# Performance work log

Hardware: AMD Instinct MI355X
Metric: run time of the kernel (lower is better)

Reference implementation:

```python
import jax, jax.numpy as jnp
import numpy as np

B, L, S, D, H = 2, 2048, 2048, 256, 8
HD = D // H  # per-head dim = 32
EPS = 1e-5


def _layernorm(x, g, b):
    m = jnp.mean(x, axis=-1, keepdims=True)
    v = jnp.mean(jnp.square(x - m), axis=-1, keepdims=True)
    return (x - m) * jax.lax.rsqrt(v + EPS) * g + b


def setup_inputs() -> dict:
    key = jax.random.key(0)
    ks = jax.random.split(key, 12)
    w = lambda k, o, i: jax.random.normal(k, (o, i), dtype=jnp.float32) * (1.0 / np.sqrt(i))
    return {
        "x": jax.random.normal(ks[0], (B, L, D), dtype=jnp.float32),
        "source": jax.random.normal(ks[1], (B, S, D), dtype=jnp.float32),
        "attn_factor": jax.random.uniform(ks[2], (B, L, S), dtype=jnp.float32),
        "Wq": w(ks[3], D, D),
        "Wk": w(ks[4], D, D),
        "Wv": w(ks[5], D, D),
        "Wm": w(ks[6], D, D),
        "W1": w(ks[7], 2 * D, 2 * D),
        "W2": w(ks[8], D, 2 * D),
        "g1": jnp.ones((D,), jnp.float32),
        "b1": jnp.zeros((D,), jnp.float32),
        "g2": jnp.ones((D,), jnp.float32),
        "b2": jnp.zeros((D,), jnp.float32),
    }


def reference(x, source, attn_factor, Wq, Wk, Wv, Wm, W1, W2, g1, b1, g2, b2):
    bs, l, d = x.shape
    s = source.shape[1]
    # projections (torch Linear: y = x @ W^T), split heads
    qw = (x @ Wq.T).reshape(bs, l, H, HD)       # [B,L,H,hd]
    kw = (source @ Wk.T).reshape(bs, s, H, HD)  # [B,S,H,hd]
    vw = (source @ Wv.T).reshape(bs, s, H, HD)  # [B,S,H,hd]
    # QK^T -> [B,L,S,H], scale, elementwise attn_factor, softmax over S
    a = jnp.einsum("nlhd,nshd->nlsh", qw, kw)
    a = a / np.sqrt(HD)
    a = a * attn_factor[:, :, :, None]
    a = jax.nn.softmax(a, axis=2)
    # AV -> [B,L,H,hd] -> merge heads
    o = jnp.einsum("nlsh,nshd->nlhd", a, vw).reshape(bs, l, d)
    message = o @ Wm.T
    message = _layernorm(message, g1, b1)
    h = jnp.concatenate([x, message], axis=2)       # [B,L,2D]
    h = jnp.maximum(h @ W1.T, 0.0)                  # ReLU MLP
    message = h @ W2.T                              # [B,L,D]
    message = _layernorm(message, g2, b2)
    return x + message
```

## Files before the change

### kernel.cpp

```cpp
#include <hip/hip_runtime.h>
#include <hip/hip_bf16.h>
#include <math.h>

#define B_  2
#define L_  2048
#define S_  2048
#define D_  256
#define H_  8
#define HD_ 32
#define ML_ (B_ * L_)
#define MS_ (B_ * S_)
#define NSPLIT 4
#define SCHUNK (S_ / NSPLIT)

typedef __attribute__((ext_vector_type(8))) short short8;
typedef __attribute__((ext_vector_type(4))) float f32x4;

__global__ __launch_bounds__(256) void convert_all(
    const float* __restrict__ x,  const float* __restrict__ src,
    const float* __restrict__ Wq, const float* __restrict__ Wk,
    const float* __restrict__ Wv, const float* __restrict__ Wm,
    const float* __restrict__ W1, const float* __restrict__ W2,
    __hip_bfloat16* xb,  __hip_bfloat16* srcb,
    __hip_bfloat16* Wqb, __hip_bfloat16* Wkb,
    __hip_bfloat16* Wvb, __hip_bfloat16* Wmb,
    __hip_bfloat16* W1b, __hip_bfloat16* W2b) {
    const size_t i4 = ((size_t)blockIdx.x * 256 + threadIdx.x) * 4;
    const float* sp; __hip_bfloat16* dp; size_t off;
    if      (i4 < 1048576) { sp = x;   dp = xb;   off = i4; }
    else if (i4 < 2097152) { sp = src; dp = srcb; off = i4 - 1048576; }
    else if (i4 < 2162688) { sp = Wq;  dp = Wqb;  off = i4 - 2097152; }
    else if (i4 < 2228224) { sp = Wk;  dp = Wkb;  off = i4 - 2162688; }
    else if (i4 < 2293760) { sp = Wv;  dp = Wvb;  off = i4 - 2228224; }
    else if (i4 < 2359296) { sp = Wm;  dp = Wmb;  off = i4 - 2293760; }
    else if (i4 < 2621440) { sp = W1;  dp = W1b;  off = i4 - 2359296; }
    else                   { sp = W2;  dp = W2b;  off = i4 - 2621440; }
    float4 v = *(const float4*)(sp + off);
    __hip_bfloat16 o0 = __float2bfloat16(v.x), o1 = __float2bfloat16(v.y);
    __hip_bfloat16 o2 = __float2bfloat16(v.z), o3 = __float2bfloat16(v.w);
    __hip_bfloat16* d = dp + off;
    d[0] = o0; d[1] = o1; d[2] = o2; d[3] = o3;
}

template <bool RELU, typename OutT>
__device__ __forceinline__ void gemm_body(const __hip_bfloat16* __restrict__ A,
                                          const __hip_bfloat16* __restrict__ A2,
                                          const __hip_bfloat16* __restrict__ Bm,
                                          OutT* __restrict__ C,
                                          int N, int K, int lda, int m0, int n0,
                                          float cscale,
                                          __hip_bfloat16 (&As)[64][72],
                                          __hip_bfloat16 (&Bs)[64][72]) {
    const int tid  = threadIdx.x;
    const int w    = tid >> 6;
    const int lane = tid & 63;
    const int colL = lane & 15;
    const int quad = lane >> 4;
    const int mh = (w & 1) * 32, nh = (w >> 1) * 32;
    const int srow = tid >> 3;
    const int scg  = (tid & 7) * 8;

    f32x4 acc[2][2] = {};

    auto loadA = [&](int p, int k0) -> short8 {
        const __hip_bfloat16* Asrc = A; int kk = k0;
        if (A2 && k0 >= 256) { Asrc = A2; kk = k0 - 256; }
        return *(const short8*)(Asrc + (size_t)(m0 + srow + p * 32) * lda + kk + scg);
    };
    auto loadB = [&](int p, int k0) -> short8 {
        return *(const short8*)(Bm + (size_t)(n0 + srow + p * 32) * K + k0 + scg);
    };

    short8 ra[2], rb[2];
#pragma unroll
    for (int p = 0; p < 2; ++p) { ra[p] = loadA(p, 0); rb[p] = loadB(p, 0); }

    for (int k0 = 0; k0 < K; k0 += 64) {
        __syncthreads();
#pragma unroll
        for (int p = 0; p < 2; ++p) {
            *(short8*)&As[srow + p * 32][scg] = ra[p];
            *(short8*)&Bs[srow + p * 32][scg] = rb[p];
        }
        __syncthreads();
        if (k0 + 64 < K) {
#pragma unroll
            for (int p = 0; p < 2; ++p) { ra[p] = loadA(p, k0 + 64); rb[p] = loadB(p, k0 + 64); }
        }
#pragma unroll
        for (int ks = 0; ks < 2; ++ks) {
            short8 af[2], bf[2];
#pragma unroll
            for (int i = 0; i < 2; ++i)
                af[i] = *(const short8*)&As[mh + i * 16 + colL][ks * 32 + quad * 8];
#pragma unroll
            for (int j = 0; j < 2; ++j)
                bf[j] = *(const short8*)&Bs[nh + j * 16 + colL][ks * 32 + quad * 8];
#pragma unroll
            for (int i = 0; i < 2; ++i)
#pragma unroll
                for (int j = 0; j < 2; ++j)
                    acc[i][j] = __builtin_amdgcn_mfma_f32_16x16x32_bf16(af[i], bf[j], acc[i][j], 0, 0, 0);
        }
    }
#pragma unroll
    for (int i = 0; i < 2; ++i)
#pragma unroll
        for (int r = 0; r < 4; ++r) {
            const size_t row = m0 + mh + i * 16 + quad * 4 + r;
#pragma unroll
            for (int j = 0; j < 2; ++j) {
                float v = acc[i][j][r] * cscale;
                if (RELU) v = fmaxf(v, 0.f);
                C[row * N + n0 + nh + j * 16 + colL] = (OutT)v;
            }
        }
}

__global__ __launch_bounds__(256) void proj_fused(const __hip_bfloat16* __restrict__ x_b,
                                                  const __hip_bfloat16* __restrict__ src_b,
                                                  const __hip_bfloat16* __restrict__ Wq_b,
                                                  const __hip_bfloat16* __restrict__ Wk_b,
                                                  const __hip_bfloat16* __restrict__ Wv_b,
                                                  __hip_bfloat16* __restrict__ Qb,
                                                  __hip_bfloat16* __restrict__ Kb,
                                                  __hip_bfloat16* __restrict__ Vtb) {
    __shared__ __hip_bfloat16 As[64][72];
    __shared__ __hip_bfloat16 Bs[64][72];
    const int id = blockIdx.x;
    if (id < 256) {
        gemm_body<false, __hip_bfloat16>(x_b, nullptr, Wq_b, Qb, 256, 256, 256,
                                         (id >> 2) * 64, (id & 3) * 64,
                                         0.17677669529663687f, As, Bs);
    } else if (id < 512) {
        const int t = id - 256;
        gemm_body<false, __hip_bfloat16>(src_b, nullptr, Wk_b, Kb, 256, 256, 256,
                                         (t >> 2) * 64, (t & 3) * 64, 1.f, As, Bs);
    } else {
        const int t = id - 512;
        const int b = t >> 7, u = t & 127;
        gemm_body<false, __hip_bfloat16>(Wv_b, nullptr, src_b + (size_t)b * S_ * D_,
                                         Vtb + (size_t)b * D_ * S_, S_, 256, 256,
                                         (u & 3) * 64, (u >> 2) * 64, 1.f, As, Bs);
    }
}

__global__ __launch_bounds__(256, 4) void attn_mfma(const __hip_bfloat16* __restrict__ Qb,
                                                    const __hip_bfloat16* __restrict__ Kb,
                                                    const __hip_bfloat16* __restrict__ Vtb,
                                                    const float* __restrict__ F,
                                                    __hip_bfloat16* __restrict__ Op,
                                                    float* __restrict__ Ll) {
    const int tid  = threadIdx.x;
    const int w    = tid >> 6;
    const int lane = tid & 63;
    const int colL = lane & 15;
    const int quad = lane >> 4;

    const int b     = blockIdx.z >> 2;
    const int split = blockIdx.z & 3;
    const int h     = blockIdx.y;
    const int qw    = blockIdx.x * 64 + w * 16;

    __shared__ __hip_bfloat16 Ks[128][40];
    __shared__ __hip_bfloat16 Vs[32][136];
    __shared__ __hip_bfloat16 Pw[4][16][72];

    const short8 aq = *(const short8*)(Qb + ((size_t)(b * L_ + qw + colL)) * D_ + h * HD_ + quad * 8);

    float lsum[4] = {0.f, 0.f, 0.f, 0.f};
    f32x4 o0 = {0.f, 0.f, 0.f, 0.f}, o1 = {0.f, 0.f, 0.f, 0.f};

    const int kr = tid >> 2, kc = (tid & 3) * 8;
    const int vr = tid >> 3, vc = (tid & 7) * 8;
    const __hip_bfloat16* kst = Kb + ((size_t)(b * S_ + kr)) * D_ + h * HD_ + kc;
    const __hip_bfloat16* vst = Vtb + (size_t)b * D_ * S_ + ((size_t)(h * HD_ + vr)) * S_ + vc;
    const float* fbase = F + ((size_t)(b * L_ + qw + quad * 4)) * S_ + colL;

    const int sbeg = split * SCHUNK, send = sbeg + SCHUNK;
    short8 rk[2], rv[2];
#pragma unroll
    for (int p = 0; p < 2; ++p) {
        rk[p] = *(const short8*)(kst + (size_t)(sbeg + p * 64) * D_);
        rv[p] = *(const short8*)(vst + sbeg + p * 64);
    }

    for (int s0 = sbeg; s0 < send; s0 += 128) {
        __syncthreads();
        *(short8*)&Ks[kr][kc]        = rk[0];
        *(short8*)&Ks[kr + 64][kc]   = rk[1];
        *(short8*)&Vs[vr][vc]        = rv[0];
        *(short8*)&Vs[vr][vc + 64]   = rv[1];
        __syncthreads();
        if (s0 + 128 < send) {
#pragma unroll
            for (int p = 0; p < 2; ++p) {
                rk[p] = *(const short8*)(kst + (size_t)(s0 + 128 + p * 64) * D_);
                rv[p] = *(const short8*)(vst + s0 + 128 + p * 64);
            }
        }
#pragma unroll
        for (int hs = 0; hs < 2; ++hs) {
            const int sh = s0 + hs * 64;
            f32x4 cc[4];
#pragma unroll
            for (int n = 0; n < 4; ++n) {
                short8 kf = *(const short8*)&Ks[hs * 64 + n * 16 + colL][quad * 8];
                f32x4 z = {0.f, 0.f, 0.f, 0.f};
                cc[n] = __builtin_amdgcn_mfma_f32_16x16x32_bf16(aq, kf, z, 0, 0, 0);
            }
#pragma unroll
            for (int n = 0; n < 4; ++n)
#pragma unroll
                for (int r = 0; r < 4; ++r) {
                    float fv = fbase[(size_t)r * S_ + sh + n * 16];
                    float p = __expf(cc[n][r] * fv);
                    lsum[r] += p;
                    Pw[w][quad * 4 + r][n * 16 + colL] = __float2bfloat16(p);
                }
            short8 a0 = *(const short8*)(&Pw[w][colL][quad * 8]);
            short8 a1 = *(const short8*)(&Pw[w][colL][32 + quad * 8]);
#pragma unroll
            for (int ks = 0; ks < 2; ++ks) {
                short8 ap = ks ? a1 : a0;
#pragma unroll
                for (int nt = 0; nt < 2; ++nt) {
                    short8 vf = *(const short8*)&Vs[nt * 16 + colL][hs * 64 + ks * 32 + quad * 8];
                    if (nt == 0) o0 = __builtin_amdgcn_mfma_f32_16x16x32_bf16(ap, vf, o0, 0, 0, 0);
                    else         o1 = __builtin_amdgcn_mfma_f32_16x16x32_bf16(ap, vf, o1, 0, 0, 0);
                }
            }
        }
    }

#pragma unroll
    for (int r = 0; r < 4; ++r) {
        float t = lsum[r];
        t += __shfl_xor(t, 1);
        t += __shfl_xor(t, 2);
        t += __shfl_xor(t, 4);
        t += __shfl_xor(t, 8);
        lsum[r] = t;
    }

#pragma unroll
    for (int r = 0; r < 4; ++r) {
        const size_t row = (size_t)(b * L_ + qw + quad * 4 + r);
        const size_t po = ((size_t)split * ML_ + row) * D_ + h * HD_;
        Op[po + colL]      = __float2bfloat16(o0[r]);
        Op[po + 16 + colL] = __float2bfloat16(o1[r]);
        if (colL == 0)
            Ll[((size_t)split * H_ + h) * ML_ + row] = lsum[r];
    }
}

__global__ __launch_bounds__(256) void mlp_fused(const __hip_bfloat16* __restrict__ Opart,
                                                 const float* __restrict__ Ll,
                                                 const __hip_bfloat16* __restrict__ x_b,
                                                 const __hip_bfloat16* __restrict__ Wm_b,
                                                 const __hip_bfloat16* __restrict__ W1_b,
                                                 const __hip_bfloat16* __restrict__ W2_b,
                                                 const float* __restrict__ g1,
                                                 const float* __restrict__ b1,
                                                 const float* __restrict__ g2,
                                                 const float* __restrict__ b2,
                                                 const float* __restrict__ x,
                                                 float* __restrict__ out) {
    __shared__ __hip_bfloat16 Bs[256][72];
    __shared__ __hip_bfloat16 As[16][72];
    __shared__ __hip_bfloat16 Acat[16][520];
    __shared__ __hip_bfloat16 Hs[16][520];
    __shared__ float gs[256], bs_[256];
    __shared__ float stats[4][16][2];
    __shared__ float Linv[16][8];

    const int tid  = threadIdx.x;
    const int w    = tid >> 6;
    const int lane = tid & 63;
    const int colL = lane & 15;
    const int quad = lane >> 4;
    const int nh   = w * 64;
    const int m0   = blockIdx.x * 16;
    const int srow = tid >> 3;
    const int scg  = (tid & 7) * 8;

    gs[tid] = g1[tid]; bs_[tid] = b1[tid];
    if (tid < 128) {
        const int row = tid >> 3, hh = tid & 7;
        float t = 0.f;
#pragma unroll
        for (int s = 0; s < NSPLIT; ++s)
            t += Ll[((size_t)s * H_ + hh) * ML_ + m0 + row];
        Linv[row][hh] = 1.f / t;
    }
    {
        const int xr = tid >> 4, xc = (tid & 15) * 16;
        *(short8*)&Acat[xr][xc]     = *(const short8*)(x_b + (size_t)(m0 + xr) * 256 + xc);
        *(short8*)&Acat[xr][xc + 8] = *(const short8*)(x_b + (size_t)(m0 + xr) * 256 + xc + 8);
    }
    __syncthreads();

    f32x4 acc[4] = {};
    auto loadA1 = [&](int k0) -> short8 {
        const float inv = Linv[srow][(k0 + scg) >> 5];
        float a[8] = {};
#pragma unroll
        for (int s = 0; s < NSPLIT; ++s) {
            short8 v = *(const short8*)(Opart + ((size_t)s * ML_ + m0 + srow) * 256 + k0 + scg);
#pragma unroll
            for (int e = 0; e < 8; ++e) {
                union { short s16; __hip_bfloat16 h; } c; c.s16 = v[e];
                a[e] += __bfloat162float(c.h);
            }
        }
        short8 outv;
#pragma unroll
        for (int e = 0; e < 8; ++e) {
            union { __hip_bfloat16 h; short s16; } c;
            c.h = __float2bfloat16(a[e] * inv);
            outv[e] = c.s16;
        }
        return outv;
    };

    {
        short8 ra = {};
        if (srow < 16) ra = loadA1(0);
        short8 rb[8];
#pragma unroll
        for (int p = 0; p < 8; ++p)
            rb[p] = *(const short8*)(Wm_b + (size_t)(srow + p * 32) * 256 + scg);
        for (int k0 = 0; k0 < 256; k0 += 64) {
            __syncthreads();
            if (srow < 16) *(short8*)&As[srow][scg] = ra;
#pragma unroll
            for (int p = 0; p < 8; ++p)
                *(short8*)&Bs[srow + p * 32][scg] = rb[p];
            __syncthreads();
            if (k0 + 64 < 256) {
                if (srow < 16) ra = loadA1(k0 + 64);
#pragma unroll
                for (int p = 0; p < 8; ++p)
                    rb[p] = *(const short8*)(Wm_b + (size_t)(srow + p * 32) * 256 + k0 + 64 + scg);
            }
#pragma unroll
            for (int ks = 0; ks < 2; ++ks) {
                short8 af = *(const short8*)&As[colL][ks * 32 + quad * 8];
#pragma unroll
                for (int j = 0; j < 4; ++j) {
                    short8 bf = *(const short8*)&Bs[nh + j * 16 + colL][ks * 32 + quad * 8];
                    acc[j] = __builtin_amdgcn_mfma_f32_16x16x32_bf16(af, bf, acc[j], 0, 0, 0);
                }
            }
        }
    }
#pragma unroll
    for (int r = 0; r < 4; ++r) {
        float s = 0.f, q = 0.f;
#pragma unroll
        for (int j = 0; j < 4; ++j) { float v = acc[j][r]; s += v; q += v * v; }
        s += __shfl_xor(s, 1); q += __shfl_xor(q, 1);
        s += __shfl_xor(s, 2); q += __shfl_xor(q, 2);
        s += __shfl_xor(s, 4); q += __shfl_xor(q, 4);
        s += __shfl_xor(s, 8); q += __shfl_xor(q, 8);
        if (colL == 0) { stats[w][quad * 4 + r][0] = s; stats[w][quad * 4 + r][1] = q; }
    }
    __syncthreads();
#pragma unroll
    for (int r = 0; r < 4; ++r) {
        const int row = quad * 4 + r;
        const float S = stats[0][row][0] + stats[1][row][0] + stats[2][row][0] + stats[3][row][0];
        const float Q = stats[0][row][1] + stats[1][row][1] + stats[2][row][1] + stats[3][row][1];
        const float mean = S * (1.f / 256.f);
        const float rstd = rsqrtf(Q * (1.f / 256.f) - mean * mean + 1e-5f);
#pragma unroll
        for (int j = 0; j < 4; ++j) {
            const int col = nh + j * 16 + colL;
            Acat[row][256 + col] = __float2bfloat16((acc[j][r] - mean) * rstd * gs[col] + bs_[col]);
        }
    }
    __syncthreads();

#pragma unroll 1
    for (int nc = 0; nc < 2; ++nc) {
#pragma unroll
        for (int j = 0; j < 4; ++j) acc[j] = (f32x4){0.f, 0.f, 0.f, 0.f};
        short8 rb[8];
#pragma unroll
        for (int p = 0; p < 8; ++p)
            rb[p] = *(const short8*)(W1_b + (size_t)(nc * 256 + srow + p * 32) * 512 + scg);
        for (int k0 = 0; k0 < 512; k0 += 64) {
            __syncthreads();
#pragma unroll
            for (int p = 0; p < 8; ++p)
                *(short8*)&Bs[srow + p * 32][scg] = rb[p];
            __syncthreads();
            if (k0 + 64 < 512) {
#pragma unroll
                for (int p = 0; p < 8; ++p)
                    rb[p] = *(const short8*)(W1_b + (size_t)(nc * 256 + srow + p * 32) * 512 + k0 + 64 + scg);
            }
#pragma unroll
            for (int ks = 0; ks < 2; ++ks) {
                short8 af = *(const short8*)&Acat[colL][k0 + ks * 32 + quad * 8];
#pragma unroll
                for (int j = 0; j < 4; ++j) {
                    short8 bf = *(const short8*)&Bs[nh + j * 16 + colL][ks * 32 + quad * 8];
                    acc[j] = __builtin_amdgcn_mfma_f32_16x16x32_bf16(af, bf, acc[j], 0, 0, 0);
                }
            }
        }
#pragma unroll
        for (int r = 0; r < 4; ++r) {
            const int row = quad * 4 + r;
#pragma unroll
            for (int j = 0; j < 4; ++j) {
                const int col = nc * 256 + nh + j * 16 + colL;
                Hs[row][col] = __float2bfloat16(fmaxf(acc[j][r], 0.f));
            }
        }
    }
    gs[tid] = g2[tid]; bs_[tid] = b2[tid];
    __syncthreads();

#pragma unroll
    for (int j = 0; j < 4; ++j) acc[j] = (f32x4){0.f, 0.f, 0.f, 0.f};
    {
        short8 rb[8];
#pragma unroll
        for (int p = 0; p < 8; ++p)
            rb[p] = *(const short8*)(W2_b + (size_t)(srow + p * 32) * 512 + scg);
        for (int k0 = 0; k0 < 512; k0 += 64) {
            __syncthreads();
#pragma unroll
            for (int p = 0; p < 8; ++p)
                *(short8*)&Bs[srow + p * 32][scg] = rb[p];
            __syncthreads();
            if (k0 + 64 < 512) {
#pragma unroll
                for (int p = 0; p < 8; ++p)
                    rb[p] = *(const short8*)(W2_b + (size_t)(srow + p * 32) * 512 + k0 + 64 + scg);
            }
#pragma unroll
            for (int ks = 0; ks < 2; ++ks) {
                short8 af = *(const short8*)&Hs[colL][k0 + ks * 32 + quad * 8];
#pragma unroll
                for (int j = 0; j < 4; ++j) {
                    short8 bf = *(const short8*)&Bs[nh + j * 16 + colL][ks * 32 + quad * 8];
                    acc[j] = __builtin_amdgcn_mfma_f32_16x16x32_bf16(af, bf, acc[j], 0, 0, 0);
                }
            }
        }
    }
#pragma unroll
    for (int r = 0; r < 4; ++r) {
        float s = 0.f, q = 0.f;
#pragma unroll
        for (int j = 0; j < 4; ++j) { float v = acc[j][r]; s += v; q += v * v; }
        s += __shfl_xor(s, 1); q += __shfl_xor(q, 1);
        s += __shfl_xor(s, 2); q += __shfl_xor(q, 2);
        s += __shfl_xor(s, 4); q += __shfl_xor(q, 4);
        s += __shfl_xor(s, 8); q += __shfl_xor(q, 8);
        if (colL == 0) { stats[w][quad * 4 + r][0] = s; stats[w][quad * 4 + r][1] = q; }
    }
    __syncthreads();
#pragma unroll
    for (int r = 0; r < 4; ++r) {
        const int row = quad * 4 + r;
        const float S = stats[0][row][0] + stats[1][row][0] + stats[2][row][0] + stats[3][row][0];
        const float Q = stats[0][row][1] + stats[1][row][1] + stats[2][row][1] + stats[3][row][1];
        const float mean = S * (1.f / 256.f);
        const float rstd = rsqrtf(Q * (1.f / 256.f) - mean * mean + 1e-5f);
        const size_t grow = (size_t)(m0 + row) * 256;
#pragma unroll
        for (int j = 0; j < 4; ++j) {
            const int col = nh + j * 16 + colL;
            out[grow + col] = (acc[j][r] - mean) * rstd * gs[col] + bs_[col] + x[grow + col];
        }
    }
}

extern "C" void kernel_launch(void* const* d_in, const int* in_sizes, int n_in,
                              void* d_out, int out_size, void* d_ws, size_t ws_size,
                              hipStream_t stream) {
    (void)in_sizes; (void)n_in; (void)out_size; (void)ws_size;
    const float* x   = (const float*)d_in[0];
    const float* src = (const float*)d_in[1];
    const float* F   = (const float*)d_in[2];
    const float* Wq  = (const float*)d_in[3];
    const float* Wk  = (const float*)d_in[4];
    const float* Wv  = (const float*)d_in[5];
    const float* Wm  = (const float*)d_in[6];
    const float* W1  = (const float*)d_in[7];
    const float* W2  = (const float*)d_in[8];
    const float* g1  = (const float*)d_in[9];
    const float* b1  = (const float*)d_in[10];
    const float* g2  = (const float*)d_in[11];
    const float* b2  = (const float*)d_in[12];
    float* out = (float*)d_out;

    char* ws = (char*)d_ws;
    __hip_bfloat16* x_b   = (__hip_bfloat16*)(ws);
    __hip_bfloat16* src_b = (__hip_bfloat16*)(ws + (2u << 20));
    __hip_bfloat16* Wq_b  = (__hip_bfloat16*)(ws + (4u << 20));
    __hip_bfloat16* Wk_b  = (__hip_bfloat16*)(ws + (4u << 20) + 131072);
    __hip_bfloat16* Wv_b  = (__hip_bfloat16*)(ws + (4u << 20) + 2 * 131072);
    __hip_bfloat16* Wm_b  = (__hip_bfloat16*)(ws + (4u << 20) + 3 * 131072);
    __hip_bfloat16* W1_b  = (__hip_bfloat16*)(ws + (4u << 20) + 4 * 131072);
    __hip_bfloat16* W2_b  = (__hip_bfloat16*)(ws + (4u << 20) + 4 * 131072 + 524288);
    __hip_bfloat16* Qb   = (__hip_bfloat16*)(ws + (6u << 20));
    __hip_bfloat16* Kb   = (__hip_bfloat16*)(ws + (8u << 20));
    __hip_bfloat16* Vtb  = (__hip_bfloat16*)(ws + (10u << 20));
    __hip_bfloat16* Opart = (__hip_bfloat16*)(ws + (14u << 20));
    float* Ll  = (float*)(ws + (22u << 20));

    dim3 blk(256);
    convert_all<<<dim3(2688), blk, 0, stream>>>(x, src, Wq, Wk, Wv, Wm, W1, W2,
                                                x_b, src_b, Wq_b, Wk_b, Wv_b, Wm_b, W1_b, W2_b);
    proj_fused<<<dim3(1024), blk, 0, stream>>>(x_b, src_b, Wq_b, Wk_b, Wv_b, Qb, Kb, Vtb);
    attn_mfma<<<dim3(L_ / 64, H_, B_ * NSPLIT), blk, 0, stream>>>(Qb, Kb, Vtb, F, Opart, Ll);
    mlp_fused<<<dim3(ML_ / 16), blk, 0, stream>>>(Opart, Ll, x_b, Wm_b, W1_b, W2_b,
                                                  g1, b1, g2, b2, x, out);
}
```

Before: 163.0 us.

## Process two heads per attention block and XOR-swizzle shared-memory tiles

Each attention block now computes two adjacent heads, so each block loads the attn_factor values, a 64-wide K tile and the V tile once and uses them for both heads. This halves the number of passes over the large fp32 attn_factor tensor, which is likely the main memory traffic. Padded shared-memory arrays are replaced by XOR-swizzled layouts for K, V and P to avoid bank conflicts without padding. The change doubles accumulator and register use per thread, which may lower occupancy. The proj_fused grid also shrinks from 1024 to 768 blocks with no visible reason.

```diff
diff --git a/kernel.cpp b/kernel.cpp
--- a/kernel.cpp
+++ b/kernel.cpp
@@ -159,98 +159,116 @@
 
     const int b     = blockIdx.z >> 2;
     const int split = blockIdx.z & 3;
-    const int h     = blockIdx.y;
+    const int by    = blockIdx.y;
     const int qw    = blockIdx.x * 64 + w * 16;
 
-    __shared__ __hip_bfloat16 Ks[128][40];
-    __shared__ __hip_bfloat16 Vs[32][136];
-    __shared__ __hip_bfloat16 Pw[4][16][72];
-
-    const short8 aq = *(const short8*)(Qb + ((size_t)(b * L_ + qw + colL)) * D_ + h * HD_ + quad * 8);
-
-    float lsum[4] = {0.f, 0.f, 0.f, 0.f};
-    f32x4 o0 = {0.f, 0.f, 0.f, 0.f}, o1 = {0.f, 0.f, 0.f, 0.f};
-
-    const int kr = tid >> 2, kc = (tid & 3) * 8;
-    const int vr = tid >> 3, vc = (tid & 7) * 8;
-    const __hip_bfloat16* kst = Kb + ((size_t)(b * S_ + kr)) * D_ + h * HD_ + kc;
-    const __hip_bfloat16* vst = Vtb + (size_t)b * D_ * S_ + ((size_t)(h * HD_ + vr)) * S_ + vc;
+    __shared__ __hip_bfloat16 Ks[128][64];
+    __shared__ __hip_bfloat16 Vs[64][128];
+    __shared__ __hip_bfloat16 Pw[4][16][64];
+
+    short8 aq2[2];
+#pragma unroll
+    for (int h2 = 0; h2 < 2; ++h2)
+        aq2[h2] = *(const short8*)(Qb + ((size_t)(b * L_ + qw + colL)) * D_ +
+                                   by * 64 + h2 * 32 + quad * 8);
+
+    float lsum[2][4] = {};
+    f32x4 o[2][2] = {};
+
+    const int kr  = tid >> 3;
+    const int kc8 = tid & 7;
+    const int vr  = tid >> 2;
+    const int vc4 = tid & 3;
+    const __hip_bfloat16* kst = Kb + ((size_t)(b * S_ + kr)) * D_ + by * 64 + kc8 * 8;
+    const __hip_bfloat16* vst = Vtb + (size_t)b * D_ * S_ + ((size_t)(by * 64 + vr)) * S_ + vc4 * 8;
     const float* fbase = F + ((size_t)(b * L_ + qw + quad * 4)) * S_ + colL;
 
     const int sbeg = split * SCHUNK, send = sbeg + SCHUNK;
-    short8 rk[2], rv[2];
-#pragma unroll
-    for (int p = 0; p < 2; ++p) {
-        rk[p] = *(const short8*)(kst + (size_t)(sbeg + p * 64) * D_);
-        rv[p] = *(const short8*)(vst + sbeg + p * 64);
+    short8 rk[4], rv[4];
+#pragma unroll
+    for (int p = 0; p < 4; ++p) {
+        rk[p] = *(const short8*)(kst + (size_t)(sbeg + p * 32) * D_);
+        rv[p] = *(const short8*)(vst + sbeg + p * 32);
     }
 
     for (int s0 = sbeg; s0 < send; s0 += 128) {
         __syncthreads();
-        *(short8*)&Ks[kr][kc]        = rk[0];
-        *(short8*)&Ks[kr + 64][kc]   = rk[1];
-        *(short8*)&Vs[vr][vc]        = rv[0];
-        *(short8*)&Vs[vr][vc + 64]   = rv[1];
+#pragma unroll
+        for (int p = 0; p < 4; ++p) {
+            *(short8*)&Ks[p * 32 + kr][(kc8 ^ (kr & 7)) * 8]           = rk[p];
+            *(short8*)&Vs[vr][((p * 4 + vc4) ^ (vr & 7)) * 8]          = rv[p];
+        }
         __syncthreads();
         if (s0 + 128 < send) {
 #pragma unroll
-            for (int p = 0; p < 2; ++p) {
-                rk[p] = *(const short8*)(kst + (size_t)(s0 + 128 + p * 64) * D_);
-                rv[p] = *(const short8*)(vst + s0 + 128 + p * 64);
+            for (int p = 0; p < 4; ++p) {
+                rk[p] = *(const short8*)(kst + (size_t)(s0 + 128 + p * 32) * D_);
+                rv[p] = *(const short8*)(vst + s0 + 128 + p * 32);
             }
         }
 #pragma unroll
         for (int hs = 0; hs < 2; ++hs) {
             const int sh = s0 + hs * 64;
-            f32x4 cc[4];
-#pragma unroll
-            for (int n = 0; n < 4; ++n) {
-                short8 kf = *(const short8*)&Ks[hs * 64 + n * 16 + colL][quad * 8];
-                f32x4 z = {0.f, 0.f, 0.f, 0.f};
-                cc[n] = __builtin_amdgcn_mfma_f32_16x16x32_bf16(aq, kf, z, 0, 0, 0);
-            }
-#pragma unroll
-            for (int n = 0; n < 4; ++n)
-#pragma unroll
-                for (int r = 0; r < 4; ++r) {
-                    float fv = fbase[(size_t)r * S_ + sh + n * 16];
-                    float p = __expf(cc[n][r] * fv);
-                    lsum[r] += p;
-                    Pw[w][quad * 4 + r][n * 16 + colL] = __float2bfloat16(p);
+#pragma unroll
+            for (int h2 = 0; h2 < 2; ++h2) {
+                f32x4 cc[4];
+#pragma unroll
+                for (int n = 0; n < 4; ++n) {
+                    short8 kf = *(const short8*)&Ks[hs * 64 + n * 16 + colL]
+                                                  [((h2 * 4 + quad) ^ (colL & 7)) * 8];
+                    f32x4 z = {0.f, 0.f, 0.f, 0.f};
+                    cc[n] = __builtin_amdgcn_mfma_f32_16x16x32_bf16(aq2[h2], kf, z, 0, 0, 0);
                 }
-            short8 a0 = *(const short8*)(&Pw[w][colL][quad * 8]);
-            short8 a1 = *(const short8*)(&Pw[w][colL][32 + quad * 8]);
-#pragma unroll
-            for (int ks = 0; ks < 2; ++ks) {
-                short8 ap = ks ? a1 : a0;
-#pragma unroll
-                for (int nt = 0; nt < 2; ++nt) {
-                    short8 vf = *(const short8*)&Vs[nt * 16 + colL][hs * 64 + ks * 32 + quad * 8];
-                    if (nt == 0) o0 = __builtin_amdgcn_mfma_f32_16x16x32_bf16(ap, vf, o0, 0, 0, 0);
-                    else         o1 = __builtin_amdgcn_mfma_f32_16x16x32_bf16(ap, vf, o1, 0, 0, 0);
+#pragma unroll
+                for (int n = 0; n < 4; ++n)
+#pragma unroll
+                    for (int r = 0; r < 4; ++r) {
+                        float fv = fbase[(size_t)r * S_ + sh + n * 16];
+                        float p = __expf(cc[n][r] * fv);
+                        lsum[h2][r] += p;
+                        const int prow = quad * 4 + r;
+                        Pw[w][prow][(n * 16 + colL) ^ ((prow & 7) << 3)] = __float2bfloat16(p);
+                    }
+                short8 a0 = *(const short8*)&Pw[w][colL][((0 + quad) ^ (colL & 7)) * 8];
+                short8 a1 = *(const short8*)&Pw[w][colL][((4 + quad) ^ (colL & 7)) * 8];
+#pragma unroll
+                for (int ks = 0; ks < 2; ++ks) {
+                    short8 ap = ks ? a1 : a0;
+#pragma unroll
+                    for (int nt = 0; nt < 2; ++nt) {
+                        short8 vf = *(const short8*)&Vs[h2 * 32 + nt * 16 + colL]
+                                                      [((hs * 8 + ks * 4 + quad) ^ (colL & 7)) * 8];
+                        o[h2][nt] = __builtin_amdgcn_mfma_f32_16x16x32_bf16(ap, vf, o[h2][nt], 0, 0, 0);
+                    }
                 }
             }
         }
     }
 
 #pragma unroll
-    for (int r = 0; r < 4; ++r) {
-        float t = lsum[r];
-        t += __shfl_xor(t, 1);
-        t += __shfl_xor(t, 2);
-        t += __shfl_xor(t, 4);
-        t += __shfl_xor(t, 8);
-        lsum[r] = t;
-    }
-
-#pragma unroll
-    for (int r = 0; r < 4; ++r) {
-        const size_t row = (size_t)(b * L_ + qw + quad * 4 + r);
-        const size_t po = ((size_t)split * ML_ + row) * D_ + h * HD_;
-        Op[po + colL]      = __float2bfloat16(o0[r]);
-        Op[po + 16 + colL] = __float2bfloat16(o1[r]);
-        if (colL == 0)
-            Ll[((size_t)split * H_ + h) * ML_ + row] = lsum[r];
+    for (int h2 = 0; h2 < 2; ++h2)
+#pragma unroll
+        for (int r = 0; r < 4; ++r) {
+            float t = lsum[h2][r];
+            t += __shfl_xor(t, 1);
+            t += __shfl_xor(t, 2);
+            t += __shfl_xor(t, 4);
+            t += __shfl_xor(t, 8);
+            lsum[h2][r] = t;
+        }
+
+#pragma unroll
+    for (int h2 = 0; h2 < 2; ++h2) {
+        const int h = by * 2 + h2;
+#pragma unroll
+        for (int r = 0; r < 4; ++r) {
+            const size_t row = (size_t)(b * L_ + qw + quad * 4 + r);
+            const size_t po = ((size_t)split * ML_ + row) * D_ + h * HD_;
+            Op[po + colL]      = __float2bfloat16(o[h2][0][r]);
+            Op[po + 16 + colL] = __float2bfloat16(o[h2][1][r]);
+            if (colL == 0)
+                Ll[((size_t)split * H_ + h) * ML_ + row] = lsum[h2][r];
+        }
     }
 }
 
@@ -517,8 +535,8 @@
     dim3 blk(256);
     convert_all<<<dim3(2688), blk, 0, stream>>>(x, src, Wq, Wk, Wv, Wm, W1, W2,
                                                 x_b, src_b, Wq_b, Wk_b, Wv_b, Wm_b, W1_b, W2_b);
-    proj_fused<<<dim3(1024), blk, 0, stream>>>(x_b, src_b, Wq_b, Wk_b, Wv_b, Qb, Kb, Vtb);
-    attn_mfma<<<dim3(L_ / 64, H_, B_ * NSPLIT), blk, 0, stream>>>(Qb, Kb, Vtb, F, Opart, Ll);
+    proj_fused<<<dim3(768), blk, 0, stream>>>(x_b, src_b, Wq_b, Wk_b, Wv_b, Qb, Kb, Vtb);
+    attn_mfma<<<dim3(L_ / 64, H_ / 2, B_ * NSPLIT), blk, 0, stream>>>(Qb, Kb, Vtb, F, Opart, Ll);
     mlp_fused<<<dim3(ML_ / 16), blk, 0, stream>>>(Opart, Ll, x_b, Wm_b, W1_b, W2_b,
                                                   g1, b1, g2, b2, x, out);
 }
```

After: 257.5 us. 1.58x slower.
